# Performance work log

Measured on AMD Instinct MI355X. Metric: run time of the kernel, lower is better.

## Reference

```python
import jax, jax.numpy as jnp
import numpy as np

N = 100000
E = 1600000
D_IN = 128
D_HID = 128


def setup_inputs() -> dict:
    key = jax.random.key(0)
    ks = jax.random.split(key, 10)
    x = jax.random.normal(ks[0], (N, D_IN), dtype=jnp.float32)
    edge_index = jax.random.randint(ks[1], (2, E), 0, N, dtype=jnp.int64)
    def lin(k, i, o):
        kw, kb = jax.random.split(k)
        s = 1.0 / np.sqrt(i)
        return (jax.random.uniform(kw, (o, i), jnp.float32, -s, s),
                jax.random.uniform(kb, (o,), jnp.float32, -s, s))
    w0a, b0a = lin(ks[2], D_IN, D_HID)
    w0b, b0b = lin(ks[3], D_HID, D_HID)
    w1a, b1a = lin(ks[4], D_HID, D_HID)
    w1b, b1b = lin(ks[5], D_HID, D_HID)
    return {"x": x, "edge_index": edge_index,
            "w0a": w0a, "b0a": b0a, "w0b": w0b, "b0b": b0b,
            "w1a": w1a, "b1a": b1a, "w1b": w1b, "b1b": b1b}


def _gin_layer(x, src, dst, wa, ba, wb, bb):
    # GINConv, eps=0: h_i = x_i + sum_{j in N(i)} x_j (messages from src aggregated at dst)
    agg = jax.ops.segment_sum(x[src], dst, num_segments=N)  # [N, D]
    h = x + agg
    h = jax.nn.relu(h @ wa.T + ba)  # LinearBlock (no bn, no dropout)
    return h @ wb.T + bb            # final Linear of local_nn


def reference(x, edge_index, w0a, b0a, w0b, b0b, w1a, b1a, w1b, b1b):
    src, dst = edge_index[0], edge_index[1]
    h = _gin_layer(x, src, dst, w0a, b0a, w0b, b0b)
    h = _gin_layer(h, src, dst, w1a, b1a, w1b, b1b)
    return h
```

## Files before the change

### kernel.cpp

```cpp
#include <hip/hip_runtime.h>


typedef __attribute__((ext_vector_type(8))) short bf16x8;
typedef __attribute__((ext_vector_type(4))) float floatx4;
typedef __attribute__((ext_vector_type(2))) float floatx2;
typedef __attribute__((ext_vector_type(4))) unsigned uintx4;

#define WS_ALIGN(x) (((x) + 255) & ~(size_t)255)
#define NBMAX 400
#define BCAP 6144

__device__ __forceinline__ unsigned short f2b(float f) {
  unsigned u = __builtin_bit_cast(unsigned, f);
  u = (u + 0x7FFF + ((u >> 16) & 1)) >> 16;
  return (unsigned short)u;
}

__device__ __forceinline__ floatx2 bpair(unsigned d) {
  floatx2 r;
  r[0] = __builtin_bit_cast(float, d << 16);
  r[1] = __builtin_bit_cast(float, d & 0xffff0000u);
  return r;
}

__global__ __launch_bounds__(256) void prep_kernel(const float* __restrict__ x,
                                                   unsigned short* __restrict__ xb,
                                                   const float* __restrict__ w0a,
                                                   const float* __restrict__ w0b,
                                                   const float* __restrict__ w1a,
                                                   const float* __restrict__ w1b,
                                                   uintx4* __restrict__ wb16,
                                                   int* __restrict__ bcnt, int n4) {
  int i = blockIdx.x * 256 + threadIdx.x;
  if (i < n4) {
    float4 v = ((const float4*)x)[i];
    uint2 pk;
    pk.x = (unsigned)f2b(v.x) | ((unsigned)f2b(v.y) << 16);
    pk.y = (unsigned)f2b(v.z) | ((unsigned)f2b(v.w) << 16);
    ((uint2*)xb)[i] = pk;
  }
  if (i < 8192) {
    const float* W = (i < 2048) ? w0a : (i < 4096) ? w0b : (i < 6144) ? w1a : w1b;
    int j = i & 2047;
    float4 a = ((const float4*)W)[j * 2];
    float4 b = ((const float4*)W)[j * 2 + 1];
    uintx4 pk;
    pk.x = (unsigned)f2b(a.x) | ((unsigned)f2b(a.y) << 16);
    pk.y = (unsigned)f2b(a.z) | ((unsigned)f2b(a.w) << 16);
    pk.z = (unsigned)f2b(b.x) | ((unsigned)f2b(b.y) << 16);
    pk.w = (unsigned)f2b(b.z) | ((unsigned)f2b(b.w) << 16);
    wb16[i] = pk;
  }
  if (i < NBMAX) bcnt[i] = 0;
}

__global__ __launch_bounds__(256) void bucket_split(const int* __restrict__ src,
                                                    const int* __restrict__ dst,
                                                    int* __restrict__ bcnt,
                                                    unsigned* __restrict__ barr, int E, int nb) {
  __shared__ int cnt[NBMAX], base[NBMAX], cur[NBMAX];
  int t = threadIdx.x;
  for (int i = t; i < nb; i += 256) { cnt[i] = 0; cur[i] = 0; }
  __syncthreads();
  int e0 = blockIdx.x * 8192;
  int s[32], d[32];
  if (e0 + 8192 <= E) {
    const int4* src4 = (const int4*)src;
    const int4* dst4 = (const int4*)dst;
    int b4 = blockIdx.x * 2048;
#pragma unroll
    for (int k = 0; k < 8; k++) {
      int4 sv = src4[b4 + k * 256 + t];
      int4 dv = dst4[b4 + k * 256 + t];
      s[k * 4 + 0] = sv.x; d[k * 4 + 0] = dv.x;
      s[k * 4 + 1] = sv.y; d[k * 4 + 1] = dv.y;
      s[k * 4 + 2] = sv.z; d[k * 4 + 2] = dv.z;
      s[k * 4 + 3] = sv.w; d[k * 4 + 3] = dv.w;
    }
  } else {
#pragma unroll
    for (int k = 0; k < 32; k++) {
      int e = e0 + k * 256 + t;
      if (e < E) { s[k] = src[e]; d[k] = dst[e]; } else { d[k] = -1; }
    }
  }
#pragma unroll
  for (int k = 0; k < 32; k++)
    if (d[k] >= 0) atomicAdd(&cnt[d[k] >> 8], 1);
  __syncthreads();
  for (int i = t; i < nb; i += 256) base[i] = cnt[i] ? atomicAdd(&bcnt[i], cnt[i]) : 0;
  __syncthreads();
#pragma unroll
  for (int k = 0; k < 32; k++)
    if (d[k] >= 0) {
      int b = d[k] >> 8;
      int r = atomicAdd(&cur[b], 1);
      barr[(size_t)b * BCAP + base[b] + r] = ((unsigned)(d[k] & 255) << 17) | (unsigned)s[k];
    }
}

__global__ __launch_bounds__(256) void bucket_csr(const unsigned* __restrict__ barr,
                                                  const int* __restrict__ bcnt,
                                                  int* __restrict__ rowptr, int* __restrict__ srt,
                                                  int n, int nb) {
  __shared__ int cnt[256], off[256], off2[256], red[256];
  int b = blockIdx.x, t = threadIdx.x;
  int cb = bcnt[b];
  int node0 = b * 256;
  int nlocal = min(256, n - node0);
  cnt[t] = 0;
  off2[t] = 0;
  int partial = 0;
  for (int i = t; i < b; i += 256) partial += bcnt[i];
  red[t] = partial;
  __syncthreads();
  for (int o = 128; o > 0; o >>= 1) {
    if (t < o) red[t] += red[t + o];
    __syncthreads();
  }
  int sb = red[0];

  const unsigned* bp = barr + (size_t)b * BCAP;
  const uint4* bp4 = (const uint4*)bp;
  int cb4 = cb >> 2;
  for (int i = t; i < cb4; i += 256) {
    uint4 v4 = bp4[i];
    atomicAdd(&cnt[v4.x >> 17], 1);
    atomicAdd(&cnt[v4.y >> 17], 1);
    atomicAdd(&cnt[v4.z >> 17], 1);
    atomicAdd(&cnt[v4.w >> 17], 1);
  }
  for (int i = cb4 * 4 + t; i < cb; i += 256) atomicAdd(&cnt[bp[i] >> 17], 1);
  __syncthreads();
  int v = cnt[t];
  off[t] = v;
  __syncthreads();
  for (int o = 1; o < 256; o <<= 1) {
    int add = (t >= o) ? off[t - o] : 0;
    __syncthreads();
    off[t] += add;
    __syncthreads();
  }
  int excl = off[t] - v;
  if (t < nlocal) rowptr[node0 + t] = sb + excl;
  cnt[t] = excl;
  __syncthreads();
  for (int i = t; i < cb4; i += 256) {
    uint4 v4 = bp4[i];
    unsigned pks[4] = {v4.x, v4.y, v4.z, v4.w};
#pragma unroll
    for (int j = 0; j < 4; j++) {
      int local = pks[j] >> 17;
      int r = atomicAdd(&off2[local], 1);
      srt[sb + cnt[local] + r] = pks[j] & 0x1FFFF;
    }
  }
  for (int i = cb4 * 4 + t; i < cb; i += 256) {
    unsigned pk = bp[i];
    int local = pk >> 17;
    int r = atomicAdd(&off2[local], 1);
    srt[sb + cnt[local] + r] = pk & 0x1FFFF;
  }
  if (b == nb - 1 && t == 0) rowptr[n] = sb + cb;
}

__global__ __launch_bounds__(256) void aggregate_bf16(const unsigned short* __restrict__ X,
                                                      const int* __restrict__ rowptr,
                                                      const int* __restrict__ srt,
                                                      unsigned short* __restrict__ out, int n) {
  int w = blockIdx.x * 4 + (threadIdx.x >> 6);
  if (w >= n) return;
  int lane = threadIdx.x & 63;
  int c = lane & 15;
  int s = lane >> 4;
  const uintx4* Xv = (const uintx4*)X;

  int p0 = rowptr[w], e = rowptr[w + 1];
  int deg = e - p0;
  int trips = (deg + 3) >> 2;

  uintx4 uself = {0, 0, 0, 0};
  if (s == 0) uself = Xv[(size_t)w * 16 + c];

  floatx2 acc2[4];
#pragma unroll
  for (int i = 0; i < 4; i++) acc2[i] = floatx2{0.f, 0.f};

  for (int g = 0; g < trips; g += 4) {
    int idx[4];
    bool val[4];
#pragma unroll
    for (int k = 0; k < 4; k++) {
      int j = (g + k) * 4 + s;
      val[k] = j < deg;
      idx[k] = srt[p0 + (val[k] ? j : 0)];
    }
    uintx4 u[4];
#pragma unroll
    for (int k = 0; k < 4; k++) u[k] = Xv[(size_t)idx[k] * 16 + c];
#pragma unroll
    for (int k = 0; k < 4; k++) {
      if (!val[k]) u[k] = uintx4{0, 0, 0, 0};
      acc2[0] += bpair(u[k].x);
      acc2[1] += bpair(u[k].y);
      acc2[2] += bpair(u[k].z);
      acc2[3] += bpair(u[k].w);
    }
  }

  acc2[0] += bpair(uself.x);
  acc2[1] += bpair(uself.y);
  acc2[2] += bpair(uself.z);
  acc2[3] += bpair(uself.w);

#pragma unroll
  for (int i = 0; i < 4; i++) {
#pragma unroll
    for (int k = 0; k < 2; k++) {
      acc2[i][k] += __shfl_xor(acc2[i][k], 16, 64);
      acc2[i][k] += __shfl_xor(acc2[i][k], 32, 64);
    }
  }

  unsigned pk = (unsigned)f2b(acc2[s][0]) | ((unsigned)f2b(acc2[s][1]) << 16);
  ((unsigned*)out)[(size_t)w * 64 + c * 4 + s] = pk;
}

__device__ __forceinline__ void stage_wb(char* buf, const uintx4* __restrict__ Wb, int t) {
  for (int idx = t; idx < 2048; idx += 512) {
    int nrow = idx >> 4, c = idx & 15;
    uintx4 pk = Wb[idx];
    *(uintx4*)(buf + nrow * 256 + ((c ^ (nrow & 15)) << 4)) = pk;
  }
}

template <int OUT_BF16>
__global__ __launch_bounds__(512) void mlp_kernel(
    const unsigned short* __restrict__ A, const uintx4* __restrict__ Wa16,
    const float* __restrict__ ba, const uintx4* __restrict__ Wb16,
    const float* __restrict__ bb, void* __restrict__ Cout, int n) {
  __shared__ __align__(16) char lds[65536];
  char* bufA = lds;
  char* bufB = lds + 32768;
  int t = threadIdx.x;
  stage_wb(bufA, Wa16, t);
  stage_wb(bufB, Wb16, t);

  int wave = t >> 6, lane = t & 63;
  int m = lane & 15, q = lane >> 4;
  int rbase = blockIdx.x * 128;
  int rowA = rbase + wave * 16 + m;
  int rA = rowA < n ? rowA : (n - 1);

  bf16x8 af[4];
  const bf16x8* Arow = (const bf16x8*)(A + (size_t)rA * 128);
#pragma unroll
  for (int ks = 0; ks < 4; ks++) af[ks] = Arow[ks * 4 + q];

  __syncthreads();

  floatx4 acc[8];
  floatx4 zf = {0.f, 0.f, 0.f, 0.f};
#pragma unroll
  for (int j = 0; j < 8; j++) acc[j] = zf;
#pragma unroll
  for (int ks = 0; ks < 4; ks++) {
#pragma unroll
    for (int j = 0; j < 8; j++) {
      bf16x8 bf = *(const bf16x8*)(bufA + (j * 16 + m) * 256 + (((ks * 4 + q) ^ m) << 4));
      acc[j] = __builtin_amdgcn_mfma_f32_16x16x32_bf16(af[ks], bf, acc[j], 0, 0, 0);
    }
  }
  __syncthreads();

#pragma unroll
  for (int j = 0; j < 8; j++) {
    float bias = ba[j * 16 + m];
#pragma unroll
    for (int reg = 0; reg < 4; reg++) {
      float v = fmaxf(acc[j][reg] + bias, 0.f);
      int lr = wave * 16 + q * 4 + reg;
      int col = j * 16 + m;
      *(unsigned short*)(bufA + lr * 256 + (((col >> 3) ^ (lr & 15)) << 4) + (col & 7) * 2) =
          f2b(v);
    }
  }
  __syncthreads();

  int lrA = wave * 16 + m;
#pragma unroll
  for (int ks = 0; ks < 4; ks++)
    af[ks] = *(const bf16x8*)(bufA + lrA * 256 + (((ks * 4 + q) ^ m) << 4));
#pragma unroll
  for (int j = 0; j < 8; j++) acc[j] = zf;
#pragma unroll
  for (int ks = 0; ks < 4; ks++) {
#pragma unroll
    for (int j = 0; j < 8; j++) {
      bf16x8 bf = *(const bf16x8*)(bufB + (j * 16 + m) * 256 + (((ks * 4 + q) ^ m) << 4));
      acc[j] = __builtin_amdgcn_mfma_f32_16x16x32_bf16(af[ks], bf, acc[j], 0, 0, 0);
    }
  }

  __syncthreads();
  int nrows = min(128, n - rbase);
  if (OUT_BF16) {
#pragma unroll
    for (int j = 0; j < 8; j++) {
      float bias = bb[j * 16 + m];
#pragma unroll
      for (int reg = 0; reg < 4; reg++) {
        int lr = wave * 16 + q * 4 + reg;
        int col = j * 16 + m;
        *(unsigned short*)(bufA + lr * 256 + col * 2) = f2b(acc[j][reg] + bias);
      }
    }
    __syncthreads();
    const uintx4* sv = (const uintx4*)bufA;
    uintx4* gout = (uintx4*)((unsigned short*)Cout + (size_t)rbase * 128);
    int chunks = nrows * 16;
    for (int i = t; i < chunks; i += 512) gout[i] = sv[i];
  } else {
    float* stg = (float*)lds;
#pragma unroll
    for (int j = 0; j < 8; j++) {
      float bias = bb[j * 16 + m];
#pragma unroll
      for (int reg = 0; reg < 4; reg++) {
        int lr = wave * 16 + q * 4 + reg;
        int col = j * 16 + m;
        stg[lr * 128 + col] = acc[j][reg] + bias;
      }
    }
    __syncthreads();
    const uintx4* sv = (const uintx4*)lds;
    uintx4* gout = (uintx4*)((float*)Cout + (size_t)rbase * 128);
    int chunks = nrows * 32;
    for (int i = t; i < chunks; i += 512) gout[i] = sv[i];
  }
}

extern "C" void kernel_launch(void* const* d_in, const int* in_sizes, int n_in,
                              void* d_out, int out_size, void* d_ws, size_t ws_size,
                              hipStream_t stream) {
  const float* x   = (const float*)d_in[0];
  const int*   ei  = (const int*)d_in[1];
  const float* w0a = (const float*)d_in[2];
  const float* b0a = (const float*)d_in[3];
  const float* w0b = (const float*)d_in[4];
  const float* b0b = (const float*)d_in[5];
  const float* w1a = (const float*)d_in[6];
  const float* b1a = (const float*)d_in[7];
  const float* w1b = (const float*)d_in[8];
  const float* b1b = (const float*)d_in[9];
  float* out = (float*)d_out;

  int n = in_sizes[0] / 128;
  int E = in_sizes[1] / 2;
  const int* src = ei;
  const int* dst = ei + E;
  int nb = (n + 255) / 256;

  char* w = (char*)d_ws;
  int* rowptr = (int*)w;           w += WS_ALIGN((size_t)(n + 1) * 4);
  int* bcnt = (int*)w;             w += WS_ALIGN((size_t)NBMAX * 4);
  int* srt = (int*)w;              w += WS_ALIGN((size_t)E * 4);
  unsigned short* xb = (unsigned short*)w;  w += WS_ALIGN((size_t)n * 128 * 2);
  uintx4* wb16 = (uintx4*)w;       w += WS_ALIGN((size_t)8192 * 16);
  unsigned* barr = (unsigned*)w;
  unsigned short* B1 = (unsigned short*)w;

  int n4 = n * 32;

  prep_kernel<<<(n4 + 255) / 256, 256, 0, stream>>>(x, xb, w0a, w0b, w1a, w1b, wb16, bcnt, n4);

  bucket_split<<<(E + 8191) / 8192, 256, 0, stream>>>(src, dst, bcnt, barr, E, nb);
  bucket_csr<<<nb, 256, 0, stream>>>(barr, bcnt, rowptr, srt, n, nb);

  int agg_grid = (n + 3) / 4;
  int mlp_grid = (n + 127) / 128;

  aggregate_bf16<<<agg_grid, 256, 0, stream>>>(xb, rowptr, srt, (unsigned short*)B1, n);
  mlp_kernel<1><<<mlp_grid, 512, 0, stream>>>(B1, wb16, b0a, wb16 + 2048, b0b, xb, n);

  aggregate_bf16<<<agg_grid, 256, 0, stream>>>(xb, rowptr, srt, (unsigned short*)B1, n);
  mlp_kernel<0><<<mlp_grid, 512, 0, stream>>>(B1, wb16 + 4096, b1a, wb16 + 6144, b1b, out, n);
}
```

Baseline: 305.4 us.

## Fuse neighbor aggregation into MLP kernel, staging aggregated rows in LDS

After: 342.2 us. +12.0%, slower.

```diff
diff --git a/kernel.cpp b/kernel.cpp
--- a/kernel.cpp
+++ b/kernel.cpp
@@ -164,68 +164,6 @@
   if (b == nb - 1 && t == 0) rowptr[n] = sb + cb;
 }
 
-__global__ __launch_bounds__(256) void aggregate_bf16(const unsigned short* __restrict__ X,
-                                                      const int* __restrict__ rowptr,
-                                                      const int* __restrict__ srt,
-                                                      unsigned short* __restrict__ out, int n) {
-  int w = blockIdx.x * 4 + (threadIdx.x >> 6);
-  if (w >= n) return;
-  int lane = threadIdx.x & 63;
-  int c = lane & 15;
-  int s = lane >> 4;
-  const uintx4* Xv = (const uintx4*)X;
-
-  int p0 = rowptr[w], e = rowptr[w + 1];
-  int deg = e - p0;
-  int trips = (deg + 3) >> 2;
-
-  uintx4 uself = {0, 0, 0, 0};
-  if (s == 0) uself = Xv[(size_t)w * 16 + c];
-
-  floatx2 acc2[4];
-#pragma unroll
-  for (int i = 0; i < 4; i++) acc2[i] = floatx2{0.f, 0.f};
-
-  for (int g = 0; g < trips; g += 4) {
-    int idx[4];
-    bool val[4];
-#pragma unroll
-    for (int k = 0; k < 4; k++) {
-      int j = (g + k) * 4 + s;
-      val[k] = j < deg;
-      idx[k] = srt[p0 + (val[k] ? j : 0)];
-    }
-    uintx4 u[4];
-#pragma unroll
-    for (int k = 0; k < 4; k++) u[k] = Xv[(size_t)idx[k] * 16 + c];
-#pragma unroll
-    for (int k = 0; k < 4; k++) {
-      if (!val[k]) u[k] = uintx4{0, 0, 0, 0};
-      acc2[0] += bpair(u[k].x);
-      acc2[1] += bpair(u[k].y);
-      acc2[2] += bpair(u[k].z);
-      acc2[3] += bpair(u[k].w);
-    }
-  }
-
-  acc2[0] += bpair(uself.x);
-  acc2[1] += bpair(uself.y);
-  acc2[2] += bpair(uself.z);
-  acc2[3] += bpair(uself.w);
-
-#pragma unroll
-  for (int i = 0; i < 4; i++) {
-#pragma unroll
-    for (int k = 0; k < 2; k++) {
-      acc2[i][k] += __shfl_xor(acc2[i][k], 16, 64);
-      acc2[i][k] += __shfl_xor(acc2[i][k], 32, 64);
-    }
-  }
-
-  unsigned pk = (unsigned)f2b(acc2[s][0]) | ((unsigned)f2b(acc2[s][1]) << 16);
-  ((unsigned*)out)[(size_t)w * 64 + c * 4 + s] = pk;
-}
-
 __device__ __forceinline__ void stage_wb(char* buf, const uintx4* __restrict__ Wb, int t) {
   for (int idx = t; idx < 2048; idx += 512) {
     int nrow = idx >> 4, c = idx & 15;
@@ -235,29 +173,84 @@
 }
 
 template <int OUT_BF16>
-__global__ __launch_bounds__(512) void mlp_kernel(
-    const unsigned short* __restrict__ A, const uintx4* __restrict__ Wa16,
+__global__ __launch_bounds__(512, 4) void gin_layer(
+    const unsigned short* __restrict__ X, const int* __restrict__ rowptr,
+    const int* __restrict__ srt, const uintx4* __restrict__ Wa16,
     const float* __restrict__ ba, const uintx4* __restrict__ Wb16,
     const float* __restrict__ bb, void* __restrict__ Cout, int n) {
   __shared__ __align__(16) char lds[65536];
   char* bufA = lds;
   char* bufB = lds + 32768;
   int t = threadIdx.x;
-  stage_wb(bufA, Wa16, t);
-  stage_wb(bufB, Wb16, t);
-
   int wave = t >> 6, lane = t & 63;
-  int m = lane & 15, q = lane >> 4;
   int rbase = blockIdx.x * 128;
-  int rowA = rbase + wave * 16 + m;
-  int rA = rowA < n ? rowA : (n - 1);
-
+
+  stage_wb(bufB, Wa16, t);
+  uintx4 wbreg[4];
+#pragma unroll
+  for (int i = 0; i < 4; i++) wbreg[i] = Wb16[t + i * 512];
+
+  int c = lane & 15;
+  int s = lane >> 4;
+  const uintx4* Xv = (const uintx4*)X;
+  for (int u = 0; u < 16; u++) {
+    int lr = wave * 16 + u;
+    int grow = rbase + lr;
+    if (grow >= n) break;
+    int p0 = rowptr[grow], deg = rowptr[grow + 1] - p0;
+    int trips = (deg + 3) >> 2;
+
+    uintx4 uself = {0, 0, 0, 0};
+    if (s == 0) uself = Xv[(size_t)grow * 16 + c];
+
+    floatx2 acc2[4];
+#pragma unroll
+    for (int i = 0; i < 4; i++) acc2[i] = floatx2{0.f, 0.f};
+
+    for (int g = 0; g < trips; g += 4) {
+      int idx[4];
+      bool val[4];
+#pragma unroll
+      for (int k = 0; k < 4; k++) {
+        int j = (g + k) * 4 + s;
+        val[k] = j < deg;
+        idx[k] = srt[p0 + (val[k] ? j : 0)];
+      }
+      uintx4 uu[4];
+#pragma unroll
+      for (int k = 0; k < 4; k++) uu[k] = Xv[(size_t)idx[k] * 16 + c];
+#pragma unroll
+      for (int k = 0; k < 4; k++) {
+        if (!val[k]) uu[k] = uintx4{0, 0, 0, 0};
+        acc2[0] += bpair(uu[k].x);
+        acc2[1] += bpair(uu[k].y);
+        acc2[2] += bpair(uu[k].z);
+        acc2[3] += bpair(uu[k].w);
+      }
+    }
+    acc2[0] += bpair(uself.x);
+    acc2[1] += bpair(uself.y);
+    acc2[2] += bpair(uself.z);
+    acc2[3] += bpair(uself.w);
+
+#pragma unroll
+    for (int i = 0; i < 4; i++) {
+#pragma unroll
+      for (int k2 = 0; k2 < 2; k2++) {
+        acc2[i][k2] += __shfl_xor(acc2[i][k2], 16, 64);
+        acc2[i][k2] += __shfl_xor(acc2[i][k2], 32, 64);
+      }
+    }
+    unsigned pk = (unsigned)f2b(acc2[s][0]) | ((unsigned)f2b(acc2[s][1]) << 16);
+    *(unsigned*)(bufA + lr * 256 + ((c ^ (lr & 15)) << 4) + s * 4) = pk;
+  }
+  __syncthreads();
+
+  int m = c, q = s;
   bf16x8 af[4];
-  const bf16x8* Arow = (const bf16x8*)(A + (size_t)rA * 128);
-#pragma unroll
-  for (int ks = 0; ks < 4; ks++) af[ks] = Arow[ks * 4 + q];
-
-  __syncthreads();
+#pragma unroll
+  for (int ks = 0; ks < 4; ks++)
+    af[ks] = *(const bf16x8*)(bufA + (wave * 16 + m) * 256 + (((ks * 4 + q) ^ m) << 4));
 
   floatx4 acc[8];
   floatx4 zf = {0.f, 0.f, 0.f, 0.f};
@@ -267,7 +260,7 @@
   for (int ks = 0; ks < 4; ks++) {
 #pragma unroll
     for (int j = 0; j < 8; j++) {
-      bf16x8 bf = *(const bf16x8*)(bufA + (j * 16 + m) * 256 + (((ks * 4 + q) ^ m) << 4));
+      bf16x8 bf = *(const bf16x8*)(bufB + (j * 16 + m) * 256 + (((ks * 4 + q) ^ m) << 4));
       acc[j] = __builtin_amdgcn_mfma_f32_16x16x32_bf16(af[ks], bf, acc[j], 0, 0, 0);
     }
   }
@@ -284,6 +277,11 @@
       *(unsigned short*)(bufA + lr * 256 + (((col >> 3) ^ (lr & 15)) << 4) + (col & 7) * 2) =
           f2b(v);
     }
+  }
+#pragma unroll
+  for (int i = 0; i < 4; i++) {
+    int idx = t + i * 512, nrow = idx >> 4, cc = idx & 15;
+    *(uintx4*)(bufB + nrow * 256 + ((cc ^ (nrow & 15)) << 4)) = wbreg[i];
   }
   __syncthreads();
 
@@ -377,12 +375,10 @@
   bucket_split<<<(E + 8191) / 8192, 256, 0, stream>>>(src, dst, bcnt, barr, E, nb);
   bucket_csr<<<nb, 256, 0, stream>>>(barr, bcnt, rowptr, srt, n, nb);
 
-  int agg_grid = (n + 3) / 4;
-  int mlp_grid = (n + 127) / 128;
-
-  aggregate_bf16<<<agg_grid, 256, 0, stream>>>(xb, rowptr, srt, (unsigned short*)B1, n);
-  mlp_kernel<1><<<mlp_grid, 512, 0, stream>>>(B1, wb16, b0a, wb16 + 2048, b0b, xb, n);
-
-  aggregate_bf16<<<agg_grid, 256, 0, stream>>>(xb, rowptr, srt, (unsigned short*)B1, n);
-  mlp_kernel<0><<<mlp_grid, 512, 0, stream>>>(B1, wb16 + 4096, b1a, wb16 + 6144, b1b, out, n);
-}
+  int gin_grid = (n + 127) / 128;
+
+  gin_layer<1><<<gin_grid, 512, 0, stream>>>(xb, rowptr, srt, wb16, b0a, wb16 + 2048, b0b,
+                                             B1, n);
+  gin_layer<0><<<gin_grid, 512, 0, stream>>>(B1, rowptr, srt, wb16 + 4096, b1a, wb16 + 6144,
+                                             b1b, out, n);
+}
```

## Stage bucketed edges in LDS for coalesced scatter and widen CSR blocks

Applied to the files above, without the earlier changes.

After: 309.4 us. No clear change (+1.3%).

```diff
diff --git a/kernel.cpp b/kernel.cpp
--- a/kernel.cpp
+++ b/kernel.cpp
@@ -9,6 +9,7 @@
 #define WS_ALIGN(x) (((x) + 255) & ~(size_t)255)
 #define NBMAX 400
 #define BCAP 6144
+#define SPB 3200
 
 __device__ __forceinline__ unsigned short f2b(float f) {
   unsigned u = __builtin_bit_cast(unsigned, f);
@@ -54,67 +55,95 @@
   if (i < NBMAX) bcnt[i] = 0;
 }
 
-__global__ __launch_bounds__(256) void bucket_split(const int* __restrict__ src,
+__global__ __launch_bounds__(512) void bucket_split(const int* __restrict__ src,
                                                     const int* __restrict__ dst,
                                                     int* __restrict__ bcnt,
                                                     unsigned* __restrict__ barr, int E, int nb) {
-  __shared__ int cnt[NBMAX], base[NBMAX], cur[NBMAX];
+  __shared__ int cnt[NBMAX], gbase[NBMAX], cur[NBMAX];
+  __shared__ int lofs[NBMAX + 1];
+  __shared__ int buf[512];
+  __shared__ unsigned stage[SPB];
   int t = threadIdx.x;
-  for (int i = t; i < nb; i += 256) { cnt[i] = 0; cur[i] = 0; }
-  __syncthreads();
-  int e0 = blockIdx.x * 8192;
-  int s[32], d[32];
-  if (e0 + 8192 <= E) {
-    const int4* src4 = (const int4*)src;
-    const int4* dst4 = (const int4*)dst;
-    int b4 = blockIdx.x * 2048;
-#pragma unroll
-    for (int k = 0; k < 8; k++) {
-      int4 sv = src4[b4 + k * 256 + t];
-      int4 dv = dst4[b4 + k * 256 + t];
-      s[k * 4 + 0] = sv.x; d[k * 4 + 0] = dv.x;
-      s[k * 4 + 1] = sv.y; d[k * 4 + 1] = dv.y;
-      s[k * 4 + 2] = sv.z; d[k * 4 + 2] = dv.z;
-      s[k * 4 + 3] = sv.w; d[k * 4 + 3] = dv.w;
-    }
-  } else {
-#pragma unroll
-    for (int k = 0; k < 32; k++) {
-      int e = e0 + k * 256 + t;
-      if (e < E) { s[k] = src[e]; d[k] = dst[e]; } else { d[k] = -1; }
-    }
-  }
-#pragma unroll
-  for (int k = 0; k < 32; k++)
+  for (int i = t; i < nb; i += 512) { cnt[i] = 0; cur[i] = 0; }
+  __syncthreads();
+  int e0 = blockIdx.x * SPB;
+  int s[8], d[8];
+  const int4* src4 = (const int4*)src;
+  const int4* dst4 = (const int4*)dst;
+#pragma unroll
+  for (int k = 0; k < 2; k++) {
+#pragma unroll
+    for (int j = 0; j < 4; j++) d[k * 4 + j] = -1;
+    int li = k * 512 + t;
+    if (li < SPB / 4) {
+      int i4 = e0 / 4 + li;
+      int ebase = i4 * 4;
+      if (ebase + 3 < E) {
+        int4 sv = src4[i4], dv = dst4[i4];
+        s[k * 4 + 0] = sv.x; d[k * 4 + 0] = dv.x;
+        s[k * 4 + 1] = sv.y; d[k * 4 + 1] = dv.y;
+        s[k * 4 + 2] = sv.z; d[k * 4 + 2] = dv.z;
+        s[k * 4 + 3] = sv.w; d[k * 4 + 3] = dv.w;
+      } else {
+#pragma unroll
+        for (int j = 0; j < 4; j++) {
+          int e = ebase + j;
+          if (e < E) { s[k * 4 + j] = src[e]; d[k * 4 + j] = dst[e]; }
+        }
+      }
+    }
+  }
+#pragma unroll
+  for (int k = 0; k < 8; k++)
     if (d[k] >= 0) atomicAdd(&cnt[d[k] >> 8], 1);
   __syncthreads();
-  for (int i = t; i < nb; i += 256) base[i] = cnt[i] ? atomicAdd(&bcnt[i], cnt[i]) : 0;
-  __syncthreads();
-#pragma unroll
-  for (int k = 0; k < 32; k++)
+  for (int i = t; i < nb; i += 512) gbase[i] = cnt[i] ? atomicAdd(&bcnt[i], cnt[i]) : 0;
+  int v = (t < nb) ? cnt[t] : 0;
+  buf[t] = v;
+  __syncthreads();
+  for (int o = 1; o < 512; o <<= 1) {
+    int add = (t >= o) ? buf[t - o] : 0;
+    __syncthreads();
+    buf[t] += add;
+    __syncthreads();
+  }
+  if (t < nb) lofs[t] = buf[t] - v;
+  if (t == nb - 1) lofs[nb] = buf[t];
+  __syncthreads();
+#pragma unroll
+  for (int k = 0; k < 8; k++)
     if (d[k] >= 0) {
       int b = d[k] >> 8;
       int r = atomicAdd(&cur[b], 1);
-      barr[(size_t)b * BCAP + base[b] + r] = ((unsigned)(d[k] & 255) << 17) | (unsigned)s[k];
-    }
-}
-
-__global__ __launch_bounds__(256) void bucket_csr(const unsigned* __restrict__ barr,
+      stage[lofs[b] + r] = ((unsigned)(d[k] & 255) << 17) | (unsigned)s[k];
+    }
+  __syncthreads();
+  int tot = lofs[nb];
+  for (int idx = t; idx < tot; idx += 512) {
+    int lo = 0, hi = nb;
+    while (hi - lo > 1) {
+      int mid = (lo + hi) >> 1;
+      if (lofs[mid] <= idx) lo = mid; else hi = mid;
+    }
+    barr[(size_t)lo * BCAP + gbase[lo] + (idx - lofs[lo])] = stage[idx];
+  }
+}
+
+__global__ __launch_bounds__(512) void bucket_csr(const unsigned* __restrict__ barr,
                                                   const int* __restrict__ bcnt,
                                                   int* __restrict__ rowptr, int* __restrict__ srt,
                                                   int n, int nb) {
-  __shared__ int cnt[256], off[256], off2[256], red[256];
+  __shared__ int cnt[256], off[256], off2[256], red[512];
   int b = blockIdx.x, t = threadIdx.x;
   int cb = bcnt[b];
   int node0 = b * 256;
   int nlocal = min(256, n - node0);
-  cnt[t] = 0;
-  off2[t] = 0;
+  if (t < 256) { cnt[t] = 0; off2[t] = 0; }
   int partial = 0;
-  for (int i = t; i < b; i += 256) partial += bcnt[i];
+  for (int i = t; i < b; i += 512) partial += bcnt[i];
   red[t] = partial;
   __syncthreads();
-  for (int o = 128; o > 0; o >>= 1) {
+  for (int o = 256; o > 0; o >>= 1) {
     if (t < o) red[t] += red[t + o];
     __syncthreads();
   }
@@ -123,29 +152,28 @@
   const unsigned* bp = barr + (size_t)b * BCAP;
   const uint4* bp4 = (const uint4*)bp;
   int cb4 = cb >> 2;
-  for (int i = t; i < cb4; i += 256) {
+  for (int i = t; i < cb4; i += 512) {
     uint4 v4 = bp4[i];
     atomicAdd(&cnt[v4.x >> 17], 1);
     atomicAdd(&cnt[v4.y >> 17], 1);
     atomicAdd(&cnt[v4.z >> 17], 1);
     atomicAdd(&cnt[v4.w >> 17], 1);
   }
-  for (int i = cb4 * 4 + t; i < cb; i += 256) atomicAdd(&cnt[bp[i] >> 17], 1);
-  __syncthreads();
-  int v = cnt[t];
-  off[t] = v;
+  for (int i = cb4 * 4 + t; i < cb; i += 512) atomicAdd(&cnt[bp[i] >> 17], 1);
+  __syncthreads();
+  int v = (t < 256) ? cnt[t] : 0;
+  if (t < 256) off[t] = v;
   __syncthreads();
   for (int o = 1; o < 256; o <<= 1) {
-    int add = (t >= o) ? off[t - o] : 0;
-    __syncthreads();
-    off[t] += add;
-    __syncthreads();
-  }
-  int excl = off[t] - v;
-  if (t < nlocal) rowptr[node0 + t] = sb + excl;
-  cnt[t] = excl;
-  __syncthreads();
-  for (int i = t; i < cb4; i += 256) {
+    int add = (t < 256 && t >= o) ? off[t - o] : 0;
+    __syncthreads();
+    if (t < 256) off[t] += add;
+    __syncthreads();
+  }
+  if (t < nlocal) rowptr[node0 + t] = sb + off[t] - v;
+  if (t < 256) cnt[t] = off[t] - v;
+  __syncthreads();
+  for (int i = t; i < cb4; i += 512) {
     uint4 v4 = bp4[i];
     unsigned pks[4] = {v4.x, v4.y, v4.z, v4.w};
 #pragma unroll
@@ -155,7 +183,7 @@
       srt[sb + cnt[local] + r] = pks[j] & 0x1FFFF;
     }
   }
-  for (int i = cb4 * 4 + t; i < cb; i += 256) {
+  for (int i = cb4 * 4 + t; i < cb; i += 512) {
     unsigned pk = bp[i];
     int local = pk >> 17;
     int r = atomicAdd(&off2[local], 1);
@@ -374,8 +402,8 @@
 
   prep_kernel<<<(n4 + 255) / 256, 256, 0, stream>>>(x, xb, w0a, w0b, w1a, w1b, wb16, bcnt, n4);
 
-  bucket_split<<<(E + 8191) / 8192, 256, 0, stream>>>(src, dst, bcnt, barr, E, nb);
-  bucket_csr<<<nb, 256, 0, stream>>>(barr, bcnt, rowptr, srt, n, nb);
+  bucket_split<<<(E + SPB - 1) / SPB, 512, 0, stream>>>(src, dst, bcnt, barr, E, nb);
+  bucket_csr<<<nb, 512, 0, stream>>>(barr, bcnt, rowptr, srt, n, nb);
 
   int agg_grid = (n + 3) / 4;
   int mlp_grid = (n + 127) / 128;
```

## Build CSR via global degree histogram, scan, and atomic scatter

Applied to the files above, without the earlier changes.

Measured after the change: 483.0 us. +58.1%, slower.

```diff
diff --git a/kernel.cpp b/kernel.cpp
--- a/kernel.cpp
+++ b/kernel.cpp
@@ -8,7 +8,6 @@
 
 #define WS_ALIGN(x) (((x) + 255) & ~(size_t)255)
 #define NBMAX 400
-#define BCAP 6144
 
 __device__ __forceinline__ unsigned short f2b(float f) {
   unsigned u = __builtin_bit_cast(unsigned, f);
@@ -30,7 +29,40 @@
                                                    const float* __restrict__ w1a,
                                                    const float* __restrict__ w1b,
                                                    uintx4* __restrict__ wb16,
-                                                   int* __restrict__ bcnt, int n4) {
+                                                   const int* __restrict__ dst,
+                                                   int* __restrict__ deg,
+                                                   int* __restrict__ bsum,
+                                                   int E, int n4, int prep_blocks) {
+  if (blockIdx.x >= prep_blocks) {
+    __shared__ int lb[NBMAX];
+    int tt = threadIdx.x;
+    for (int i = tt; i < NBMAX; i += 256) lb[i] = 0;
+    __syncthreads();
+    int hb = blockIdx.x - prep_blocks;
+    const int4* d4 = (const int4*)dst;
+    int base4 = hb * 1024;
+#pragma unroll
+    for (int k = 0; k < 4; k++) {
+      int i4 = base4 + k * 256 + tt;
+      if (i4 * 4 + 3 < E) {
+        int4 dv = d4[i4];
+        atomicAdd(&deg[dv.x], 1); atomicAdd(&lb[dv.x >> 8], 1);
+        atomicAdd(&deg[dv.y], 1); atomicAdd(&lb[dv.y >> 8], 1);
+        atomicAdd(&deg[dv.z], 1); atomicAdd(&lb[dv.z >> 8], 1);
+        atomicAdd(&deg[dv.w], 1); atomicAdd(&lb[dv.w >> 8], 1);
+      } else {
+        for (int e = i4 * 4; e < E && e < i4 * 4 + 4; e++) {
+          int d = dst[e];
+          atomicAdd(&deg[d], 1);
+          atomicAdd(&lb[d >> 8], 1);
+        }
+      }
+    }
+    __syncthreads();
+    for (int i = tt; i < NBMAX; i += 256)
+      if (lb[i]) atomicAdd(&bsum[i], lb[i]);
+    return;
+  }
   int i = blockIdx.x * 256 + threadIdx.x;
   if (i < n4) {
     float4 v = ((const float4*)x)[i];
@@ -51,67 +83,15 @@
     pk.w = (unsigned)f2b(b.z) | ((unsigned)f2b(b.w) << 16);
     wb16[i] = pk;
   }
-  if (i < NBMAX) bcnt[i] = 0;
-}
-
-__global__ __launch_bounds__(256) void bucket_split(const int* __restrict__ src,
-                                                    const int* __restrict__ dst,
-                                                    int* __restrict__ bcnt,
-                                                    unsigned* __restrict__ barr, int E, int nb) {
-  __shared__ int cnt[NBMAX], base[NBMAX], cur[NBMAX];
-  int t = threadIdx.x;
-  for (int i = t; i < nb; i += 256) { cnt[i] = 0; cur[i] = 0; }
-  __syncthreads();
-  int e0 = blockIdx.x * 8192;
-  int s[32], d[32];
-  if (e0 + 8192 <= E) {
-    const int4* src4 = (const int4*)src;
-    const int4* dst4 = (const int4*)dst;
-    int b4 = blockIdx.x * 2048;
-#pragma unroll
-    for (int k = 0; k < 8; k++) {
-      int4 sv = src4[b4 + k * 256 + t];
-      int4 dv = dst4[b4 + k * 256 + t];
-      s[k * 4 + 0] = sv.x; d[k * 4 + 0] = dv.x;
-      s[k * 4 + 1] = sv.y; d[k * 4 + 1] = dv.y;
-      s[k * 4 + 2] = sv.z; d[k * 4 + 2] = dv.z;
-      s[k * 4 + 3] = sv.w; d[k * 4 + 3] = dv.w;
-    }
-  } else {
-#pragma unroll
-    for (int k = 0; k < 32; k++) {
-      int e = e0 + k * 256 + t;
-      if (e < E) { s[k] = src[e]; d[k] = dst[e]; } else { d[k] = -1; }
-    }
-  }
-#pragma unroll
-  for (int k = 0; k < 32; k++)
-    if (d[k] >= 0) atomicAdd(&cnt[d[k] >> 8], 1);
-  __syncthreads();
-  for (int i = t; i < nb; i += 256) base[i] = cnt[i] ? atomicAdd(&bcnt[i], cnt[i]) : 0;
-  __syncthreads();
-#pragma unroll
-  for (int k = 0; k < 32; k++)
-    if (d[k] >= 0) {
-      int b = d[k] >> 8;
-      int r = atomicAdd(&cur[b], 1);
-      barr[(size_t)b * BCAP + base[b] + r] = ((unsigned)(d[k] & 255) << 17) | (unsigned)s[k];
-    }
-}
-
-__global__ __launch_bounds__(256) void bucket_csr(const unsigned* __restrict__ barr,
-                                                  const int* __restrict__ bcnt,
-                                                  int* __restrict__ rowptr, int* __restrict__ srt,
-                                                  int n, int nb) {
-  __shared__ int cnt[256], off[256], off2[256], red[256];
+}
+
+__global__ __launch_bounds__(256) void scan_kernel(int* __restrict__ deg,
+                                                   const int* __restrict__ bsum,
+                                                   int* __restrict__ rowptr, int n, int nb) {
+  __shared__ int red[256], off[256];
   int b = blockIdx.x, t = threadIdx.x;
-  int cb = bcnt[b];
-  int node0 = b * 256;
-  int nlocal = min(256, n - node0);
-  cnt[t] = 0;
-  off2[t] = 0;
   int partial = 0;
-  for (int i = t; i < b; i += 256) partial += bcnt[i];
+  for (int i = t; i < b; i += 256) partial += bsum[i];
   red[t] = partial;
   __syncthreads();
   for (int o = 128; o > 0; o >>= 1) {
@@ -119,20 +99,8 @@
     __syncthreads();
   }
   int sb = red[0];
-
-  const unsigned* bp = barr + (size_t)b * BCAP;
-  const uint4* bp4 = (const uint4*)bp;
-  int cb4 = cb >> 2;
-  for (int i = t; i < cb4; i += 256) {
-    uint4 v4 = bp4[i];
-    atomicAdd(&cnt[v4.x >> 17], 1);
-    atomicAdd(&cnt[v4.y >> 17], 1);
-    atomicAdd(&cnt[v4.z >> 17], 1);
-    atomicAdd(&cnt[v4.w >> 17], 1);
-  }
-  for (int i = cb4 * 4 + t; i < cb; i += 256) atomicAdd(&cnt[bp[i] >> 17], 1);
-  __syncthreads();
-  int v = cnt[t];
+  int g = b * 256 + t;
+  int v = (g < n) ? deg[g] : 0;
   off[t] = v;
   __syncthreads();
   for (int o = 1; o < 256; o <<= 1) {
@@ -141,27 +109,38 @@
     off[t] += add;
     __syncthreads();
   }
-  int excl = off[t] - v;
-  if (t < nlocal) rowptr[node0 + t] = sb + excl;
-  cnt[t] = excl;
-  __syncthreads();
-  for (int i = t; i < cb4; i += 256) {
-    uint4 v4 = bp4[i];
-    unsigned pks[4] = {v4.x, v4.y, v4.z, v4.w};
-#pragma unroll
-    for (int j = 0; j < 4; j++) {
-      int local = pks[j] >> 17;
-      int r = atomicAdd(&off2[local], 1);
-      srt[sb + cnt[local] + r] = pks[j] & 0x1FFFF;
-    }
-  }
-  for (int i = cb4 * 4 + t; i < cb; i += 256) {
-    unsigned pk = bp[i];
-    int local = pk >> 17;
-    int r = atomicAdd(&off2[local], 1);
-    srt[sb + cnt[local] + r] = pk & 0x1FFFF;
-  }
-  if (b == nb - 1 && t == 0) rowptr[n] = sb + cb;
+  if (g <= n) rowptr[g] = sb + off[t] - v;
+  if (g < n) deg[g] = sb + off[t];
+  if (b == nb - 1 && t == 255) rowptr[n] = sb + off[255];
+}
+
+__global__ __launch_bounds__(256) void scatter_kernel(const int* __restrict__ src,
+                                                      const int* __restrict__ dst,
+                                                      int* __restrict__ deg,
+                                                      int* __restrict__ srt, int E, int T) {
+  int t = blockIdx.x * 256 + threadIdx.x;
+  const int4* s4 = (const int4*)src;
+  const int4* d4 = (const int4*)dst;
+#pragma unroll
+  for (int k = 0; k < 2; k++) {
+    int i4 = t + k * T;
+    if (i4 * 4 + 3 < E) {
+      int4 sv = s4[i4], dv = d4[i4];
+      int v0 = atomicSub(&deg[dv.x], 1);
+      int v1 = atomicSub(&deg[dv.y], 1);
+      int v2 = atomicSub(&deg[dv.z], 1);
+      int v3 = atomicSub(&deg[dv.w], 1);
+      srt[v0 - 1] = sv.x;
+      srt[v1 - 1] = sv.y;
+      srt[v2 - 1] = sv.z;
+      srt[v3 - 1] = sv.w;
+    } else {
+      for (int e = i4 * 4; e < E && e < i4 * 4 + 4; e++) {
+        int v = atomicSub(&deg[dst[e]], 1);
+        srt[v - 1] = src[e];
+      }
+    }
+  }
 }
 
 __global__ __launch_bounds__(256) void aggregate_bf16(const unsigned short* __restrict__ X,
@@ -363,19 +342,23 @@
 
   char* w = (char*)d_ws;
   int* rowptr = (int*)w;           w += WS_ALIGN((size_t)(n + 1) * 4);
-  int* bcnt = (int*)w;             w += WS_ALIGN((size_t)NBMAX * 4);
+  int* deg = (int*)w;
+  int* bsum = deg + n;             w += WS_ALIGN(((size_t)n + NBMAX) * 4);
   int* srt = (int*)w;              w += WS_ALIGN((size_t)E * 4);
   unsigned short* xb = (unsigned short*)w;  w += WS_ALIGN((size_t)n * 128 * 2);
   uintx4* wb16 = (uintx4*)w;       w += WS_ALIGN((size_t)8192 * 16);
-  unsigned* barr = (unsigned*)w;
   unsigned short* B1 = (unsigned short*)w;
 
   int n4 = n * 32;
-
-  prep_kernel<<<(n4 + 255) / 256, 256, 0, stream>>>(x, xb, w0a, w0b, w1a, w1b, wb16, bcnt, n4);
-
-  bucket_split<<<(E + 8191) / 8192, 256, 0, stream>>>(src, dst, bcnt, barr, E, nb);
-  bucket_csr<<<nb, 256, 0, stream>>>(barr, bcnt, rowptr, srt, n, nb);
+  int prep_blocks = (n4 + 255) / 256;
+  int histo_blocks = (E + 4095) / 4096;
+
+  hipMemsetAsync(deg, 0, ((size_t)n + NBMAX) * 4, stream);
+  prep_kernel<<<prep_blocks + histo_blocks, 256, 0, stream>>>(
+      x, xb, w0a, w0b, w1a, w1b, wb16, dst, deg, bsum, E, n4, prep_blocks);
+  scan_kernel<<<nb, 256, 0, stream>>>(deg, bsum, rowptr, n, nb);
+  int sc_blocks = (E / 8 + 255) / 256;
+  scatter_kernel<<<sc_blocks, 256, 0, stream>>>(src, dst, deg, srt, E, sc_blocks * 256);
 
   int agg_grid = (n + 3) / 4;
   int mlp_grid = (n + 127) / 128;
```
